# Performance work log

Measured on AMD Instinct MI355X. Metric: run time of the kernel, lower is better.

## Reference

```python
import jax, jax.numpy as jnp
import numpy as np

N = 50000      # nodes
E = 800000     # edges (avg degree 16)
IN = 64        # in_channels
H = 128        # hidden_channels
OUT = 64       # out_channels
G = 64         # number of graphs in batch


def setup_inputs() -> dict:
    key = jax.random.key(0)
    ks = jax.random.split(key, 16)
    x = jax.random.normal(ks[0], (N, IN), dtype=jnp.float32)
    edge_index = jax.random.randint(ks[1], (2, E), 0, N, dtype=jnp.int64)
    batch = jnp.sort(jax.random.randint(ks[2], (N,), 0, G, dtype=jnp.int64))
    s = 0.05
    return {
        "x": x,
        "edge_index": edge_index,
        "batch": batch,
        # SAGEConv1: out = aggr @ W_l + x @ W_r + b
        "W1l": jax.random.normal(ks[3], (IN, H), dtype=jnp.float32) * s,
        "W1r": jax.random.normal(ks[4], (IN, H), dtype=jnp.float32) * s,
        "b1": jnp.zeros((H,), dtype=jnp.float32),
        # SAGEConv2
        "W2l": jax.random.normal(ks[5], (H, H), dtype=jnp.float32) * s,
        "W2r": jax.random.normal(ks[6], (H, H), dtype=jnp.float32) * s,
        "b2": jnp.zeros((H,), dtype=jnp.float32),
        # MLP head
        "W3": jax.random.normal(ks[7], (H, H), dtype=jnp.float32) * s,
        "b3": jnp.zeros((H,), dtype=jnp.float32),
        "W4": jax.random.normal(ks[8], (H, OUT), dtype=jnp.float32) * s,
        "b4": jnp.zeros((OUT,), dtype=jnp.float32),
    }


def sage_conv(x, src, dst, Wl, Wr, b, n_nodes):
    # mean-aggregate neighbor (source) features onto target nodes
    msgs = x[src]                                            # [E, d] gather
    agg = jax.ops.segment_sum(msgs, dst, num_segments=n_nodes)
    cnt = jax.ops.segment_sum(jnp.ones((src.shape[0],), x.dtype), dst,
                              num_segments=n_nodes)
    agg = agg / jnp.maximum(cnt, 1.0)[:, None]               # mean, 0 if no nbrs
    return agg @ Wl + x @ Wr + b


def reference(x, edge_index, batch, W1l, W1r, b1, W2l, W2r, b2, W3, b3, W4, b4):
    src, dst = edge_index[0], edge_index[1]
    n = x.shape[0]
    h = jax.nn.elu(sage_conv(x, src, dst, W1l, W1r, b1, n))   # dropout: eval mode (no-op)
    h = jax.nn.elu(sage_conv(h, src, dst, W2l, W2r, b2, n))
    # global mean pool per graph
    gsum = jax.ops.segment_sum(h, batch, num_segments=G)
    gcnt = jax.ops.segment_sum(jnp.ones((n,), h.dtype), batch, num_segments=G)
    gmean = gsum / jnp.maximum(gcnt, 1.0)[:, None]
    # global max pool per graph
    gmax = jax.ops.segment_max(h, batch, num_segments=G)
    pool = gmean + gmax                                       # [G, H]
    out = jax.nn.relu(pool @ W3 + b3) @ W4 + b4               # [G, OUT]
    return out
```

## Files before the change

### kernel.cpp

```cpp
#include <hip/hip_runtime.h>
#include <math.h>

constexpr int HDIM = 128;
constexpr int GRAPHS = 64;
constexpr int OUTD = 64;
constexpr int POOL_SPLIT = 8;
constexpr int BK_SHIFT = 7;
constexpr int BK_NODES = 1 << BK_SHIFT;
constexpr int BK_CAP   = 2560;

typedef __attribute__((ext_vector_type(8))) short bf16x8;
typedef __attribute__((ext_vector_type(8))) unsigned short us8;
typedef __attribute__((ext_vector_type(4))) unsigned short us4;
typedef __attribute__((ext_vector_type(4))) float f32x4;

__device__ inline float bf2f(unsigned short u) {
  return __uint_as_float(((unsigned int)u) << 16);
}
__device__ inline unsigned short f2bf(float x) {
  unsigned int u = __float_as_uint(x);
  return (unsigned short)((u + 0x7FFF + ((u >> 16) & 1)) >> 16);
}

__device__ inline void atomicMaxF(float* addr, float v) {
  if (v >= 0.0f) atomicMax((int*)addr, __float_as_int(v));
  else           atomicMin((unsigned int*)addr, __float_as_uint(v));
}

__device__ inline void pack_body(const float* __restrict__ W, unsigned short* __restrict__ P,
                                 int K, int tid) {
  int lane = tid & 63, frag = tid >> 6;
  int t = frag >> 3, ct = frag & 7;
  int kb = t * 32 + (lane >> 4) * 8;
  int col = ct * 16 + (lane & 15);
  us8 o;
#pragma unroll
  for (int i = 0; i < 8; i++) o[i] = f2bf(W[(size_t)(kb + i) * HDIM + col]);
  *(us8*)(P + (size_t)tid * 8) = o;
}

__global__ __launch_bounds__(256) void prep_k(
    const float* __restrict__ x, unsigned short* __restrict__ x_b, int nx4,
    const float* __restrict__ W1l, const float* __restrict__ W1r,
    const float* __restrict__ W2l, const float* __restrict__ W2r,
    unsigned short* w1l_p, unsigned short* w1r_p,
    unsigned short* w2l_p, unsigned short* w2r_p,
    int* __restrict__ gcnt, int nbk,
    float* __restrict__ gsum, float* __restrict__ gmax) {
  const int b = blockIdx.x, t = threadIdx.x;
  if (b < 4)        pack_body(W1l, w1l_p, 64,  b * 256 + t);
  else if (b < 8)   pack_body(W1r, w1r_p, 64,  (b - 4) * 256 + t);
  else if (b < 16)  pack_body(W2l, w2l_p, 128, (b - 8) * 256 + t);
  else if (b < 24)  pack_body(W2r, w2r_p, 128, (b - 16) * 256 + t);
  else if (b == 24) { for (int i = t; i < nbk; i += 256) gcnt[i] = 0; }
  else if (b == 25) {
    for (int i = t; i < GRAPHS * HDIM; i += 256) { gsum[i] = 0.0f; gmax[i] = -INFINITY; }
  } else {
    for (int i = (b - 26) * 256 + t; i < nx4; i += 256 * 256) {
      float4 v = ((const float4*)x)[i];
      us4 o = { f2bf(v.x), f2bf(v.y), f2bf(v.z), f2bf(v.w) };
      *((us4*)x_b + i) = o;
    }
  }
}

__global__ __launch_bounds__(256) void partition_k(const int* __restrict__ src,
                                                   const int* __restrict__ dst,
                                                   int* __restrict__ gcnt,
                                                   int* __restrict__ ebuf,
                                                   int E, int nbk) {
  __shared__ int hist[512];
  __shared__ int lcur[512];
  __shared__ int rbase[512];
  const int t = threadIdx.x;
  int tile = (E + gridDim.x - 1) / gridDim.x;
  int e0 = blockIdx.x * tile;
  int e1 = min(E, e0 + tile);
  for (int i = t; i < 512; i += 256) { hist[i] = 0; lcur[i] = 0; }
  __syncthreads();
  for (int e = e0 + t; e < e1; e += 256)
    atomicAdd(&hist[dst[e] >> BK_SHIFT], 1);
  __syncthreads();
  for (int b = t; b < nbk; b += 256)
    if (hist[b] > 0) rbase[b] = atomicAdd(&gcnt[b], hist[b]);
  __syncthreads();
  for (int e = e0 + t; e < e1; e += 256) {
    int d = dst[e];
    int b = d >> BK_SHIFT;
    int slot = rbase[b] + atomicAdd(&lcur[b], 1);
    if (slot < BK_CAP)
      ebuf[(size_t)b * BK_CAP + slot] = ((d & (BK_NODES - 1)) << 20) | src[e];
  }
}

__global__ __launch_bounds__(128) void scan_bounds_k(const int* __restrict__ gcnt,
                                                     int* __restrict__ bbase, int B,
                                                     const int* __restrict__ batch,
                                                     int* __restrict__ gstart, int n) {
  const int t = threadIdx.x;
  if (t < 64) {
    const int lane = t;
    int carry = 0;
    for (int base = 0; base < B; base += 64) {
      int i = base + lane;
      int v = (i < B) ? gcnt[i] : 0;
      int incl = v;
#pragma unroll
      for (int d = 1; d < 64; d <<= 1) {
        int u = __shfl_up(incl, d, 64);
        if (lane >= d) incl += u;
      }
      if (i < B) bbase[i] = carry + incl - v;
      carry += __shfl(incl, 63, 64);
    }
    if (lane == 0) bbase[B] = carry;
  } else {
    int g = t - 64;
    int lo = 0, hi = n;
    while (lo < hi) {
      int mid = (lo + hi) >> 1;
      if (batch[mid] < g) lo = mid + 1; else hi = mid;
    }
    gstart[g] = lo;
    if (g == 0) gstart[GRAPHS] = n;
  }
}

__global__ __launch_bounds__(256) void perm_build_k(const int* __restrict__ ebuf,
                                                    const int* __restrict__ gcnt,
                                                    const int* __restrict__ bbase,
                                                    int* __restrict__ offs,
                                                    int* __restrict__ perm, int n) {
  __shared__ int st[BK_CAP];
  __shared__ int perm_st[BK_CAP];
  __shared__ int nh[BK_NODES];
  __shared__ int excl_s[BK_NODES];
  __shared__ int lc[BK_NODES];
  const int b = blockIdx.x;
  const int t = threadIdx.x;
  const int nodeBase = b << BK_SHIFT;
  const int cnt = min(gcnt[b], BK_CAP);
  const int bb = bbase[b];
  for (int i = t; i < BK_NODES; i += 256) nh[i] = 0;
  __syncthreads();
  for (int i = t; i < cnt; i += 256) {
    int e = ebuf[(size_t)b * BK_CAP + i];
    st[i] = e;
    atomicAdd(&nh[e >> 20], 1);
  }
  __syncthreads();
  if (t < 64) {
    int v0 = nh[t];
    int incl = v0;
#pragma unroll
    for (int d = 1; d < 64; d <<= 1) {
      int u = __shfl_up(incl, d, 64);
      if (t >= d) incl += u;
    }
    excl_s[t] = incl - v0;
    int tot0 = __shfl(incl, 63, 64);
    int v1 = nh[64 + t];
    int incl1 = v1;
#pragma unroll
    for (int d = 1; d < 64; d <<= 1) {
      int u = __shfl_up(incl1, d, 64);
      if (t >= d) incl1 += u;
    }
    excl_s[64 + t] = tot0 + incl1 - v1;
  }
  __syncthreads();
  for (int i = t; i < BK_NODES; i += 256) {
    int idx = nodeBase + i;
    if (idx <= n) offs[idx] = bb + excl_s[i];
  }
  for (int i = t; i < BK_NODES; i += 256) lc[i] = excl_s[i];
  __syncthreads();
  for (int i = t; i < cnt; i += 256) {
    int e = st[i];
    int slot = atomicAdd(&lc[e >> 20], 1);
    perm_st[slot] = e & 0xFFFFF;
  }
  __syncthreads();
  for (int i = t; i < cnt; i += 256) perm[bb + i] = perm_st[i];
}

template<int K, int ROWS>
__global__ __launch_bounds__(256) void sage_fused_k(
    const unsigned short* __restrict__ feat,
    const int* __restrict__ offs, const int* __restrict__ perm,
    const unsigned short* __restrict__ B0, const unsigned short* __restrict__ B1,
    const float* __restrict__ bias, unsigned short* __restrict__ out, int n) {
  constexpr int NT = K / 32;
  constexpr int C8 = K / 8;
  constexpr int SR = K + 24;
  constexpr int RPP = 256 / C8;
  constexpr int PASSES = (ROWS + RPP - 1) / RPP;
  constexpr int RT = ROWS / 16;
  constexpr int WPR = 4 / RT;
  constexpr int CTW = 8 / WPR;
  __shared__ unsigned short a_lds[ROWS * SR];
  const int t = threadIdx.x;
  const int rowBase = blockIdx.x * ROWS;

#pragma unroll
  for (int p = 0; p < PASSES; p++) {
    int lr = p * RPP + t / C8;
    int c8 = t % C8;
    int row = rowBase + lr;
    if (lr < ROWS && row < n) {
      int s = offs[row], e = offs[row + 1];
      float acc[8] = {0.f, 0.f, 0.f, 0.f, 0.f, 0.f, 0.f, 0.f};
      const unsigned short* fb = feat + c8 * 8;
      int j = s;
      for (; j + 3 < e; j += 4) {
        int r0 = perm[j], r1 = perm[j + 1], r2 = perm[j + 2], r3 = perm[j + 3];
        us8 v0 = *(const us8*)(fb + (size_t)r0 * K);
        us8 v1 = *(const us8*)(fb + (size_t)r1 * K);
        us8 v2 = *(const us8*)(fb + (size_t)r2 * K);
        us8 v3 = *(const us8*)(fb + (size_t)r3 * K);
#pragma unroll
        for (int q = 0; q < 8; q++)
          acc[q] += (bf2f(v0[q]) + bf2f(v1[q])) + (bf2f(v2[q]) + bf2f(v3[q]));
      }
      for (; j < e; j++) {
        int r = perm[j];
        us8 v = *(const us8*)(fb + (size_t)r * K);
#pragma unroll
        for (int q = 0; q < 8; q++) acc[q] += bf2f(v[q]);
      }
      float sc = 1.0f / fmaxf((float)(e - s), 1.0f);
      us8 o;
#pragma unroll
      for (int q = 0; q < 8; q++) o[q] = f2bf(acc[q] * sc);
      *(us8*)(a_lds + lr * SR + c8 * 8) = o;
    }
  }
  __syncthreads();

  const int lane = t & 63;
  const int w = t >> 6;
  const int rh = w / WPR;
  const int cw = w % WPR;
  const int row0 = rowBase + rh * 16;
  if (row0 >= n) return;
  const int l16 = lane & 15, lhi = lane >> 4;
  f32x4 acc[CTW];
#pragma unroll
  for (int cc = 0; cc < CTW; cc++) acc[cc] = (f32x4){0.f, 0.f, 0.f, 0.f};
  const unsigned short* al = a_lds + (rh * 16 + l16) * SR + lhi * 8;
  const unsigned short* ag = feat + (size_t)(row0 + l16) * K + lhi * 8;
#pragma unroll
  for (int t2 = 0; t2 < NT; t2++) {
    bf16x8 afA = *(const bf16x8*)(al + t2 * 32);
    bf16x8 afS = *(const bf16x8*)(ag + t2 * 32);
#pragma unroll
    for (int cc = 0; cc < CTW; cc++) {
      int ct = cw * CTW + cc;
      bf16x8 b0 = *(const bf16x8*)(B0 + ((size_t)(t2 * 8 + ct) * 64 + lane) * 8);
      acc[cc] = __builtin_amdgcn_mfma_f32_16x16x32_bf16(afA, b0, acc[cc], 0, 0, 0);
      bf16x8 b1 = *(const bf16x8*)(B1 + ((size_t)(t2 * 8 + ct) * 64 + lane) * 8);
      acc[cc] = __builtin_amdgcn_mfma_f32_16x16x32_bf16(afS, b1, acc[cc], 0, 0, 0);
    }
  }
#pragma unroll
  for (int cc = 0; cc < CTW; cc++) {
    int col = (cw * CTW + cc) * 16 + l16;
    float bs = bias[col];
#pragma unroll
    for (int i = 0; i < 4; i++) {
      int row = row0 + lhi * 4 + i;
      if (row < n) {
        float v = acc[cc][i] + bs;
        v = (v > 0.f) ? v : expm1f(v);
        out[(size_t)row * HDIM + col] = f2bf(v);
      }
    }
  }
}

__global__ __launch_bounds__(256) void pool2_k(const unsigned short* __restrict__ h,
                                               const int* __restrict__ gstart,
                                               float* __restrict__ gsum,
                                               float* __restrict__ gmax) {
  __shared__ float rs[16][HDIM];
  __shared__ float rm[16][HDIM];
  const int g = blockIdx.x / POOL_SPLIT;
  const int slice = blockIdx.x % POOL_SPLIT;
  const int t = threadIdx.x;
  const int r = t >> 4;
  const int c8 = t & 15;
  const int s = gstart[g], e = gstart[g + 1];
  const int cnt = e - s;
  if (cnt <= 0) return;
  int chunk = (cnt + POOL_SPLIT - 1) / POOL_SPLIT;
  int ns = s + slice * chunk;
  int ne = min(e, ns + chunk);
  float sum[8] = {0.f, 0.f, 0.f, 0.f, 0.f, 0.f, 0.f, 0.f};
  float mx[8];
#pragma unroll
  for (int q = 0; q < 8; q++) mx[q] = -INFINITY;
  for (int node = ns + r; node < ne; node += 16) {
    us8 v = *(const us8*)(h + (size_t)node * HDIM + c8 * 8);
#pragma unroll
    for (int q = 0; q < 8; q++) {
      float f = bf2f(v[q]);
      sum[q] += f;
      mx[q] = fmaxf(mx[q], f);
    }
  }
#pragma unroll
  for (int q = 0; q < 8; q++) { rs[r][c8 * 8 + q] = sum[q]; rm[r][c8 * 8 + q] = mx[q]; }
  __syncthreads();
  if (t < HDIM) {
    float ssum = 0.f, smx = -INFINITY;
#pragma unroll
    for (int i = 0; i < 16; i++) { ssum += rs[i][t]; smx = fmaxf(smx, rm[i][t]); }
    atomicAdd(&gsum[g * HDIM + t], ssum);
    atomicMaxF(&gmax[g * HDIM + t], smx);
  }
}

__global__ __launch_bounds__(128) void head_k(
    const float* __restrict__ gsum, const float* __restrict__ gmax,
    const int* __restrict__ gstart,
    const float* __restrict__ W3, const float* __restrict__ b3,
    const float* __restrict__ W4, const float* __restrict__ b4,
    float* __restrict__ out) {
  __shared__ float pool_s[HDIM];
  __shared__ float t1_s[HDIM];
  int g = blockIdx.x, c = threadIdx.x;
  float cntf = (float)(gstart[g + 1] - gstart[g]);
  float ic = 1.0f / fmaxf(cntf, 1.0f);
  pool_s[c] = gsum[g * HDIM + c] * ic + gmax[g * HDIM + c];
  __syncthreads();
  float acc = b3[c];
  for (int k = 0; k < HDIM; k++) acc += pool_s[k] * W3[k * HDIM + c];
  t1_s[c] = fmaxf(acc, 0.0f);
  __syncthreads();
  if (c < OUTD) {
    float acc2 = b4[c];
    for (int k = 0; k < HDIM; k++) acc2 += t1_s[k] * W4[k * OUTD + c];
    out[g * OUTD + c] = acc2;
  }
}

extern "C" void kernel_launch(void* const* d_in, const int* in_sizes, int n_in,
                              void* d_out, int out_size, void* d_ws, size_t ws_size,
                              hipStream_t stream) {
  const float* x     = (const float*)d_in[0];
  const int*   ei    = (const int*)d_in[1];
  const int*   batch = (const int*)d_in[2];
  const float* W1l = (const float*)d_in[3];
  const float* W1r = (const float*)d_in[4];
  const float* b1  = (const float*)d_in[5];
  const float* W2l = (const float*)d_in[6];
  const float* W2r = (const float*)d_in[7];
  const float* b2  = (const float*)d_in[8];
  const float* W3  = (const float*)d_in[9];
  const float* b3  = (const float*)d_in[10];
  const float* W4  = (const float*)d_in[11];
  const float* b4  = (const float*)d_in[12];

  const int N  = in_sizes[2];
  const int E  = in_sizes[1] / 2;
  const int IN = in_sizes[0] / N;
  const int* src = ei;
  const int* dst = ei + E;
  const int NBK = (N + BK_NODES - 1) / BK_NODES;

  char* ws = (char*)d_ws;
  size_t off = 0;
  auto alloc = [&](size_t bytes) { void* p = ws + off; off += (bytes + 255) & ~(size_t)255; return p; };
  int*  offs  = (int*)alloc((size_t)(N + 1) * 4);
  int*  perm  = (int*)alloc((size_t)E * 4);
  int*  gcnt  = (int*)alloc((size_t)NBK * 4);
  int*  bbase = (int*)alloc((size_t)(NBK + 1) * 4);
  int*  ebuf  = (int*)alloc((size_t)NBK * BK_CAP * 4);
  unsigned short* x_b   = (unsigned short*)alloc((size_t)N * IN * 2);
  unsigned short* h1_b  = (unsigned short*)alloc((size_t)N * HDIM * 2);
  unsigned short* h2_b  = (unsigned short*)alloc((size_t)N * HDIM * 2);
  unsigned short* w1l_p = (unsigned short*)alloc((size_t)IN * HDIM * 2);
  unsigned short* w1r_p = (unsigned short*)alloc((size_t)IN * HDIM * 2);
  unsigned short* w2l_p = (unsigned short*)alloc((size_t)HDIM * HDIM * 2);
  unsigned short* w2r_p = (unsigned short*)alloc((size_t)HDIM * HDIM * 2);
  float* gsum = (float*)alloc((size_t)GRAPHS * HDIM * 4);
  float* gmax = (float*)alloc((size_t)GRAPHS * HDIM * 4);
  int* gstart = (int*)alloc((size_t)(GRAPHS + 1) * 4);
  (void)ws_size; (void)n_in; (void)out_size;

  prep_k<<<282, 256, 0, stream>>>(x, x_b, N * IN / 4, W1l, W1r, W2l, W2r,
                                  w1l_p, w1r_p, w2l_p, w2r_p, gcnt, NBK, gsum, gmax);

  partition_k<<<256, 256, 0, stream>>>(src, dst, gcnt, ebuf, E, NBK);
  scan_bounds_k<<<1, 128, 0, stream>>>(gcnt, bbase, NBK, batch, gstart, N);
  perm_build_k<<<NBK, 256, 0, stream>>>(ebuf, gcnt, bbase, offs, perm, N);

  sage_fused_k<64, 32><<<(N + 31) / 32, 256, 0, stream>>>(x_b, offs, perm, w1l_p, w1r_p, b1, h1_b, N);

  sage_fused_k<128, 16><<<(N + 15) / 16, 256, 0, stream>>>(h1_b, offs, perm, w2l_p, w2r_p, b2, h2_b, N);

  pool2_k<<<GRAPHS * POOL_SPLIT, 256, 0, stream>>>(h2_b, gstart, gsum, gmax);
  head_k<<<GRAPHS, 128, 0, stream>>>(gsum, gmax, gstart, W3, b3, W4, b4, (float*)d_out);
}
```

Baseline: 120.2 us.

## Fuse global mean/max pooling into second SAGE layer epilogue

The second SAGE layer now pools its ELU output per graph straight from an LDS tile. It does run-length grouping over the sorted batch ids and issues atomic add and atomic max into gsum/gmax, so the separate pool kernel and the h2 buffer round trip are gone. The second layer's row tile also grows from 16 to 32 rows per block. This removes one launch and a full N×128 bf16 write and read, but adds many more global atomics (per block and column for each graph segment) and changes occupancy and LDS use for layer 2.

Measured after the change: 112.2 us. 1.07x faster.

```diff
diff --git a/kernel.cpp b/kernel.cpp
--- a/kernel.cpp
+++ b/kernel.cpp
@@ -4,7 +4,6 @@
 constexpr int HDIM = 128;
 constexpr int GRAPHS = 64;
 constexpr int OUTD = 64;
-constexpr int POOL_SPLIT = 8;
 constexpr int BK_SHIFT = 7;
 constexpr int BK_NODES = 1 << BK_SHIFT;
 constexpr int BK_CAP   = 2560;
@@ -184,12 +183,14 @@
   for (int i = t; i < cnt; i += 256) perm[bb + i] = perm_st[i];
 }
 
-template<int K, int ROWS>
+template<int K, int ROWS, bool POOL>
 __global__ __launch_bounds__(256) void sage_fused_k(
     const unsigned short* __restrict__ feat,
     const int* __restrict__ offs, const int* __restrict__ perm,
     const unsigned short* __restrict__ B0, const unsigned short* __restrict__ B1,
-    const float* __restrict__ bias, unsigned short* __restrict__ out, int n) {
+    const float* __restrict__ bias, unsigned short* __restrict__ out,
+    const int* __restrict__ batch, float* __restrict__ gsum, float* __restrict__ gmax,
+    int n) {
   constexpr int NT = K / 32;
   constexpr int C8 = K / 8;
   constexpr int SR = K + 24;
@@ -198,7 +199,9 @@
   constexpr int RT = ROWS / 16;
   constexpr int WPR = 4 / RT;
   constexpr int CTW = 8 / WPR;
+  constexpr int PSR = HDIM + 8;
   __shared__ unsigned short a_lds[ROWS * SR];
+  __shared__ int batch_s[ROWS];
   const int t = threadIdx.x;
   const int rowBase = blockIdx.x * ROWS;
 
@@ -235,6 +238,10 @@
       *(us8*)(a_lds + lr * SR + c8 * 8) = o;
     }
   }
+  if (POOL && t < ROWS) {
+    int row = rowBase + t;
+    batch_s[t] = (row < n) ? batch[row] : -1;
+  }
   __syncthreads();
 
   const int lane = t & 63;
@@ -242,13 +249,12 @@
   const int rh = w / WPR;
   const int cw = w % WPR;
   const int row0 = rowBase + rh * 16;
-  if (row0 >= n) return;
   const int l16 = lane & 15, lhi = lane >> 4;
   f32x4 acc[CTW];
 #pragma unroll
   for (int cc = 0; cc < CTW; cc++) acc[cc] = (f32x4){0.f, 0.f, 0.f, 0.f};
   const unsigned short* al = a_lds + (rh * 16 + l16) * SR + lhi * 8;
-  const unsigned short* ag = feat + (size_t)(row0 + l16) * K + lhi * 8;
+  const unsigned short* ag = feat + (size_t)min(row0 + l16, n - 1) * K + lhi * 8;
 #pragma unroll
   for (int t2 = 0; t2 < NT; t2++) {
     bf16x8 afA = *(const bf16x8*)(al + t2 * 32);
@@ -262,61 +268,60 @@
       acc[cc] = __builtin_amdgcn_mfma_f32_16x16x32_bf16(afS, b1, acc[cc], 0, 0, 0);
     }
   }
-#pragma unroll
-  for (int cc = 0; cc < CTW; cc++) {
-    int col = (cw * CTW + cc) * 16 + l16;
-    float bs = bias[col];
-#pragma unroll
-    for (int i = 0; i < 4; i++) {
-      int row = row0 + lhi * 4 + i;
-      if (row < n) {
+
+  if constexpr (!POOL) {
+#pragma unroll
+    for (int cc = 0; cc < CTW; cc++) {
+      int col = (cw * CTW + cc) * 16 + l16;
+      float bs = bias[col];
+#pragma unroll
+      for (int i = 0; i < 4; i++) {
+        int row = row0 + lhi * 4 + i;
+        if (row < n) {
+          float v = acc[cc][i] + bs;
+          v = (v > 0.f) ? v : expm1f(v);
+          out[(size_t)row * HDIM + col] = f2bf(v);
+        }
+      }
+    }
+  } else {
+    __syncthreads();
+    unsigned short* ptile = a_lds;
+#pragma unroll
+    for (int cc = 0; cc < CTW; cc++) {
+      int col = (cw * CTW + cc) * 16 + l16;
+      float bs = bias[col];
+#pragma unroll
+      for (int i = 0; i < 4; i++) {
+        int rl = rh * 16 + lhi * 4 + i;
         float v = acc[cc][i] + bs;
         v = (v > 0.f) ? v : expm1f(v);
-        out[(size_t)row * HDIM + col] = f2bf(v);
-      }
-    }
-  }
-}
-
-__global__ __launch_bounds__(256) void pool2_k(const unsigned short* __restrict__ h,
-                                               const int* __restrict__ gstart,
-                                               float* __restrict__ gsum,
-                                               float* __restrict__ gmax) {
-  __shared__ float rs[16][HDIM];
-  __shared__ float rm[16][HDIM];
-  const int g = blockIdx.x / POOL_SPLIT;
-  const int slice = blockIdx.x % POOL_SPLIT;
-  const int t = threadIdx.x;
-  const int r = t >> 4;
-  const int c8 = t & 15;
-  const int s = gstart[g], e = gstart[g + 1];
-  const int cnt = e - s;
-  if (cnt <= 0) return;
-  int chunk = (cnt + POOL_SPLIT - 1) / POOL_SPLIT;
-  int ns = s + slice * chunk;
-  int ne = min(e, ns + chunk);
-  float sum[8] = {0.f, 0.f, 0.f, 0.f, 0.f, 0.f, 0.f, 0.f};
-  float mx[8];
-#pragma unroll
-  for (int q = 0; q < 8; q++) mx[q] = -INFINITY;
-  for (int node = ns + r; node < ne; node += 16) {
-    us8 v = *(const us8*)(h + (size_t)node * HDIM + c8 * 8);
-#pragma unroll
-    for (int q = 0; q < 8; q++) {
-      float f = bf2f(v[q]);
-      sum[q] += f;
-      mx[q] = fmaxf(mx[q], f);
-    }
-  }
-#pragma unroll
-  for (int q = 0; q < 8; q++) { rs[r][c8 * 8 + q] = sum[q]; rm[r][c8 * 8 + q] = mx[q]; }
-  __syncthreads();
-  if (t < HDIM) {
-    float ssum = 0.f, smx = -INFINITY;
-#pragma unroll
-    for (int i = 0; i < 16; i++) { ssum += rs[i][t]; smx = fmaxf(smx, rm[i][t]); }
-    atomicAdd(&gsum[g * HDIM + t], ssum);
-    atomicMaxF(&gmax[g * HDIM + t], smx);
+        ptile[rl * PSR + col] = f2bf(v);
+      }
+    }
+    __syncthreads();
+    int c = t & 127;
+    int half = t >> 7;
+    float sum = 0.0f, mx = -INFINITY;
+    int gc = -1;
+    for (int r = half * (ROWS / 2); r < (half + 1) * (ROWS / 2); r++) {
+      int g = batch_s[r];
+      if (g < 0) continue;
+      float v = bf2f(ptile[r * PSR + c]);
+      if (g != gc) {
+        if (gc >= 0) {
+          atomicAdd(&gsum[gc * HDIM + c], sum);
+          atomicMaxF(&gmax[gc * HDIM + c], mx);
+        }
+        gc = g; sum = 0.0f; mx = -INFINITY;
+      }
+      sum += v;
+      mx = fmaxf(mx, v);
+    }
+    if (gc >= 0) {
+      atomicAdd(&gsum[gc * HDIM + c], sum);
+      atomicMaxF(&gmax[gc * HDIM + c], mx);
+    }
   }
 }
 
@@ -378,7 +383,6 @@
   int*  ebuf  = (int*)alloc((size_t)NBK * BK_CAP * 4);
   unsigned short* x_b   = (unsigned short*)alloc((size_t)N * IN * 2);
   unsigned short* h1_b  = (unsigned short*)alloc((size_t)N * HDIM * 2);
-  unsigned short* h2_b  = (unsigned short*)alloc((size_t)N * HDIM * 2);
   unsigned short* w1l_p = (unsigned short*)alloc((size_t)IN * HDIM * 2);
   unsigned short* w1r_p = (unsigned short*)alloc((size_t)IN * HDIM * 2);
   unsigned short* w2l_p = (unsigned short*)alloc((size_t)HDIM * HDIM * 2);
@@ -395,10 +399,11 @@
   scan_bounds_k<<<1, 128, 0, stream>>>(gcnt, bbase, NBK, batch, gstart, N);
   perm_build_k<<<NBK, 256, 0, stream>>>(ebuf, gcnt, bbase, offs, perm, N);
 
-  sage_fused_k<64, 32><<<(N + 31) / 32, 256, 0, stream>>>(x_b, offs, perm, w1l_p, w1r_p, b1, h1_b, N);
-
-  sage_fused_k<128, 16><<<(N + 15) / 16, 256, 0, stream>>>(h1_b, offs, perm, w2l_p, w2r_p, b2, h2_b, N);
-
-  pool2_k<<<GRAPHS * POOL_SPLIT, 256, 0, stream>>>(h2_b, gstart, gsum, gmax);
+  sage_fused_k<64, 32, false><<<(N + 31) / 32, 256, 0, stream>>>(
+      x_b, offs, perm, w1l_p, w1r_p, b1, h1_b, nullptr, nullptr, nullptr, N);
+
+  sage_fused_k<128, 32, true><<<(N + 31) / 32, 256, 0, stream>>>(
+      h1_b, offs, perm, w2l_p, w2r_p, b2, nullptr, batch, gsum, gmax, N);
+
   head_k<<<GRAPHS, 128, 0, stream>>>(gsum, gmax, gstart, W3, b3, W4, b4, (float*)d_out);
 }
```
